# Kernel tuning notes

Hardware: AMD Instinct MI355X
Metric: run time of the kernel (lower is better)

Reference implementation:

```python
import jax, jax.numpy as jnp
import numpy as np

ALPHA = 300.0   # attractor_alpha
N_ATT = 16      # n_attractors
MIN_D = 0.001
MAX_D = 10.0


def _resize_bilinear_ac(x, out_h, out_w):
    """Bilinear resize with align_corners=True on trailing (H, W) dims of [B,C,h,w]."""
    h, w = x.shape[-2], x.shape[-1]
    ys = jnp.arange(out_h, dtype=jnp.float32) * ((h - 1) / max(out_h - 1, 1))
    xs = jnp.arange(out_w, dtype=jnp.float32) * ((w - 1) / max(out_w - 1, 1))
    y0 = jnp.floor(ys).astype(jnp.int32); y1 = jnp.minimum(y0 + 1, h - 1)
    x0 = jnp.floor(xs).astype(jnp.int32); x1 = jnp.minimum(x0 + 1, w - 1)
    wy = (ys - y0.astype(jnp.float32))[:, None]   # [out_h, 1]
    wx = (xs - x0.astype(jnp.float32))[None, :]   # [1, out_w]
    v00 = x[..., y0[:, None], x0[None, :]]
    v01 = x[..., y0[:, None], x1[None, :]]
    v10 = x[..., y1[:, None], x0[None, :]]
    v11 = x[..., y1[:, None], x1[None, :]]
    top = v00 * (1 - wx) + v01 * wx
    bot = v10 * (1 - wx) + v11 * wx
    return top * (1 - wy) + bot * wy


def setup_inputs() -> dict:
    key = jax.random.key(0)
    k = jax.random.split(key, 7)
    B, C, H, W = 4, 128, 192, 192
    n_bins = 64
    x = jax.random.normal(k[0], (B, C, H, W), dtype=jnp.float32)
    prev_bin = jax.random.uniform(k[1], (B, n_bins, H // 2, W // 2), dtype=jnp.float32)
    prev_bin_embedding = jax.random.normal(k[2], (B, C, H // 2, W // 2), dtype=jnp.float32)
    w1 = jax.random.normal(k[3], (128, 128), dtype=jnp.float32) * 0.05
    b1 = jnp.zeros((128,), dtype=jnp.float32)
    w2 = jax.random.normal(k[4], (2 * N_ATT, 128), dtype=jnp.float32) * 0.05
    b2 = jnp.zeros((2 * N_ATT,), dtype=jnp.float32)
    return {"x": x, "prev_bin": prev_bin, "prev_bin_embedding": prev_bin_embedding,
            "w1": w1, "b1": b1, "w2": w2, "b2": b2}


def reference(x, prev_bin, prev_bin_embedding, w1, b1, w2, b2):
    B, C, H, W = x.shape
    # add (interpolated) previous bin embedding
    pe = _resize_bilinear_ac(prev_bin_embedding, H, W)
    h = x + pe
    # per-pixel MLP (two 1x1 convs)
    h = jax.nn.relu(jnp.einsum('bchw,oc->bohw', h, w1) + b1[:, None, None])
    att = jax.nn.relu(jnp.einsum('bchw,oc->bohw', h, w2) + b2[:, None, None]) + 0.001
    # [B, n_attractors, 2, H, W] -> take normed attractor points
    att = att.reshape(B, N_ATT, 2, H, W)[:, :, 0]          # [B, nA, H, W]
    # upsample previous bin centers to feature resolution
    bc = _resize_bilinear_ac(prev_bin, H, W)               # [B, nB, H, W]
    # broadcast-subtract + inverse attractor + mean over attractors
    dx = att[:, :, None, :, :] - bc[:, None, :, :, :]      # [B, nA, nB, H, W]
    delta_c = jnp.mean(dx / (1.0 + ALPHA * dx * dx), axis=1)  # gamma = 2
    bin_new_centers = bc + delta_c
    bin_centers = (MAX_D - MIN_D) * bin_new_centers + MIN_D
    bin_centers = jnp.clip(jnp.sort(bin_centers, axis=1), MIN_D, MAX_D)
    return bin_new_centers, bin_centers
```

## Files before the change

### kernel.cpp

```cpp
#include <hip/hip_runtime.h>

constexpr int Bc = 4, Cc = 128, Hc = 192, Wc = 192;
constexpr int HI = 96, WI = 96;
constexpr int NB = 64;
constexpr int NA = 16;
constexpr float SCL = 95.0f / 191.0f;

typedef __attribute__((ext_vector_type(8))) short bf16x8;
typedef __attribute__((ext_vector_type(4))) float f32x4;

__device__ __forceinline__ unsigned short f2bf(float f) {
  unsigned u = __builtin_bit_cast(unsigned, f);
  unsigned r = (u + 0x7FFFu + ((u >> 16) & 1u)) >> 16;
  return (unsigned short)r;
}
__device__ __forceinline__ float rcp_fast(float r) {
#if defined(__has_builtin)
#if __has_builtin(__builtin_amdgcn_rcpf)
  return __builtin_amdgcn_rcpf(r);
#else
  return 1.0f / r;
#endif
#else
  return 1.0f / r;
#endif
}

__global__ __launch_bounds__(256) void k_prep(
    const float* __restrict__ w1, const float* __restrict__ w2,
    unsigned short* __restrict__ w1bf, unsigned short* __restrict__ w2bf)
{
  const int t = blockIdx.x * 256 + threadIdx.x;
  if (t < 16384) {
    w1bf[t] = f2bf(w1[t]);
  } else {
    const int u = t - 16384;
    const int j = u >> 7, c = u & 127;
    w2bf[u] = f2bf(w2[(2 * j) * 128 + c]);
  }
}

__global__ __launch_bounds__(256, 8) void k_att(
    const float* __restrict__ x, const float* __restrict__ pbe,
    const unsigned short* __restrict__ w1bf, const float* __restrict__ b1,
    const unsigned short* __restrict__ w2bf, const float* __restrict__ b2,
    float* __restrict__ att)
{
  constexpr int PH = 136;
  constexpr int RP = 37;
  __shared__ __align__(16) unsigned char smem[128 * RP * 4];
  float*          row_s = (float*)smem;
  unsigned short* a1_s  = (unsigned short*)smem;

  const int tid = threadIdx.x;
  const int xg0 = blockIdx.x * 64;
  const int y = blockIdx.y;
  const int b = blockIdx.z;

  const float ysf = y * SCL;
  const int y0 = (int)ysf;
  const int y1 = min(y0 + 1, HI - 1);
  const float wy = ysf - (float)y0;
  const int xi0 = (int)(xg0 * SCL);

  const int lane = tid & 63;
  const int wv = tid >> 6;
  const int ln = lane & 15;
  const int qd = lane >> 4;
  const int m0 = wv * 16;

  const int px = m0 + ln;
  const int xg = xg0 + px;
  const float xsf = (float)xg * SCL;
  const int x0i = (int)xsf;
  const float wx = xsf - (float)x0i;
  const int xl = x0i - xi0;

  float xr[32];
  #pragma unroll
  for (int kt = 0; kt < 4; ++kt) {
    #pragma unroll
    for (int j = 0; j < 8; ++j) {
      const int c = kt * 32 + qd * 8 + j;
      xr[kt * 8 + j] = x[((size_t)(b * Cc + c) * Hc + y) * Wc + xg];
    }
  }

  #pragma unroll
  for (int i = 0; i < 18; ++i) {
    const int f = tid + 256 * i;
    const int c = f / 36;
    const int xi = f - c * 36;
    const int xgl = min(xi0 + xi, WI - 1);
    const float* p = pbe + (size_t)(b * Cc + c) * (HI * WI);
    const float top = p[y0 * WI + xgl];
    const float bot = p[y1 * WI + xgl];
    row_s[c * RP + xi] = top + wy * (bot - top);
  }
  __syncthreads();

  bf16x8 af[4];
  #pragma unroll
  for (int kt = 0; kt < 4; ++kt) {
    #pragma unroll
    for (int j = 0; j < 8; ++j) {
      const int c = kt * 32 + qd * 8 + j;
      const float v0 = row_s[c * RP + xl];
      const float v1 = row_s[c * RP + xl + 1];
      af[kt][j] = (short)f2bf(xr[kt * 8 + j] + v0 + wx * (v1 - v0));
    }
  }
  __syncthreads();

  f32x4 acc[8];
  #pragma unroll
  for (int nt = 0; nt < 8; ++nt) acc[nt] = f32x4{0.f, 0.f, 0.f, 0.f};
  #pragma unroll
  for (int nt = 0; nt < 8; ++nt) {
    #pragma unroll
    for (int kt = 0; kt < 4; ++kt) {
      const bf16x8 bf = *(const bf16x8*)&w1bf[(nt * 16 + ln) * 128 + kt * 32 + qd * 8];
      acc[nt] = __builtin_amdgcn_mfma_f32_16x16x32_bf16(af[kt], bf, acc[nt], 0, 0, 0);
    }
  }

  #pragma unroll
  for (int nt = 0; nt < 8; ++nt) {
    const int n = nt * 16 + ln;
    const float bias = b1[n];
    #pragma unroll
    for (int r = 0; r < 4; ++r) {
      const int m = m0 + qd * 4 + r;
      a1_s[m * PH + n] = f2bf(fmaxf(acc[nt][r] + bias, 0.f));
    }
  }

  f32x4 acc2 = f32x4{0.f, 0.f, 0.f, 0.f};
  #pragma unroll
  for (int kt = 0; kt < 4; ++kt) {
    const bf16x8 a2 = *(const bf16x8*)&a1_s[(m0 + ln) * PH + kt * 32 + qd * 8];
    const bf16x8 b2f = *(const bf16x8*)&w2bf[ln * 128 + kt * 32 + qd * 8];
    acc2 = __builtin_amdgcn_mfma_f32_16x16x32_bf16(a2, b2f, acc2, 0, 0, 0);
  }
  const float bias2 = b2[2 * ln];
  #pragma unroll
  for (int r = 0; r < 4; ++r) {
    const int opx = m0 + qd * 4 + r;
    const float v = fmaxf(acc2[r] + bias2, 0.f) + 0.001f;
    att[((size_t)((b * Hc + y) * Wc) + xg0 + opx) * NA + ln] = v;
  }
}

__global__ __launch_bounds__(192, 2) void k_bins(
    const float* __restrict__ pb, const float* __restrict__ att,
    float* __restrict__ out0, float* __restrict__ out1)
{
  __shared__ __align__(16) float row_s[NB][WI];

  const int tid = threadIdx.x;
  const int y = blockIdx.x;
  const int b = blockIdx.y;

  const float ysf = y * SCL;
  const int y0 = (int)ysf;
  const int y1 = min(y0 + 1, HI - 1);
  const float wy = ysf - (float)y0;

  float am[16];
  {
    const float4* ap = (const float4*)(att + ((size_t)((b * Hc + y) * Wc) + tid) * NA);
    const float4 a0 = ap[0], a1 = ap[1], a2 = ap[2], a3 = ap[3];
    am[0] = a0.x;  am[1] = a0.y;  am[2] = a0.z;  am[3] = a0.w;
    am[4] = a1.x;  am[5] = a1.y;  am[6] = a1.z;  am[7] = a1.w;
    am[8] = a2.x;  am[9] = a2.y;  am[10] = a2.z; am[11] = a2.w;
    am[12] = a3.x; am[13] = a3.y; am[14] = a3.z; am[15] = a3.w;
  }

  #pragma unroll
  for (int i = 0; i < 8; ++i) {
    const int u = tid + 192 * i;
    const int k = u / 24;
    const int g = u - k * 24;
    const float* base = pb + (size_t)(b * NB + k) * (HI * WI);
    const float4 t4 = *(const float4*)&base[y0 * WI + g * 4];
    const float4 b4 = *(const float4*)&base[y1 * WI + g * 4];
    float4 r;
    r.x = t4.x + wy * (b4.x - t4.x);
    r.y = t4.y + wy * (b4.y - t4.y);
    r.z = t4.z + wy * (b4.z - t4.z);
    r.w = t4.w + wy * (b4.w - t4.w);
    *(float4*)&row_s[k][g * 4] = r;
  }
  __syncthreads();

  const float xsf = tid * SCL;
  const int x0 = (int)xsf;
  const float wx = xsf - (float)x0;

  const size_t obase = (size_t)(b * NB) * (Hc * Wc) + (size_t)y * Wc + tid;
  float v[NB];

  #pragma unroll
  for (int kb = 0; kb < NB; kb += 4) {
    float bc[4], dl[4];
    #pragma unroll
    for (int q = 0; q < 4; ++q) {
      const int k = kb + q;
      const float v0 = row_s[k][x0], v1 = row_s[k][x0 + 1];
      bc[q] = v0 + wx * (v1 - v0);
      dl[q] = 0.f;
    }
    #pragma unroll
    for (int j = 0; j < NA; ++j) {
      const float a = am[j];
      #pragma unroll
      for (int q = 0; q < 4; ++q) {
        const float d = a - bc[q];
        const float rq = fmaf(300.f * d, d, 1.f);
        dl[q] = fmaf(d, rcp_fast(rq), dl[q]);
      }
    }
    #pragma unroll
    for (int q = 0; q < 4; ++q) {
      const float bnc = fmaf(dl[q], 1.f / 16.f, bc[q]);
      out0[obase + (size_t)(kb + q) * (Hc * Wc)] = bnc;
      v[kb + q] = fmaf(9.999f, bnc, 0.001f);
    }
  }

  #pragma unroll
  for (int size = 2; size <= NB; size <<= 1) {
    #pragma unroll
    for (int stride = size >> 1; stride >= 1; stride >>= 1) {
      #pragma unroll
      for (int i = 0; i < NB; ++i) {
        if ((i & stride) == 0) {
          const int j = i | stride;
          const bool asc = ((i & size) == 0);
          const float a = v[i], c = v[j];
          const float lo = fminf(a, c), hi = fmaxf(a, c);
          v[i] = asc ? lo : hi;
          v[j] = asc ? hi : lo;
        }
      }
    }
  }

  #pragma unroll
  for (int k = 0; k < NB; ++k) {
    out1[obase + (size_t)k * (Hc * Wc)] = fminf(fmaxf(v[k], 0.001f), 10.0f);
  }
}

extern "C" void kernel_launch(void* const* d_in, const int* in_sizes, int n_in,
                              void* d_out, int out_size, void* d_ws, size_t ws_size,
                              hipStream_t stream) {
  const float* x   = (const float*)d_in[0];
  const float* pb  = (const float*)d_in[1];
  const float* pbe = (const float*)d_in[2];
  const float* w1  = (const float*)d_in[3];
  const float* b1  = (const float*)d_in[4];
  const float* w2  = (const float*)d_in[5];
  const float* b2  = (const float*)d_in[6];

  float* out0 = (float*)d_out;
  float* out1 = out0 + (size_t)Bc * NB * Hc * Wc;

  unsigned short* w1bf = (unsigned short*)d_ws;
  unsigned short* w2bf = w1bf + 16384;
  float* att = (float*)((char*)d_ws + 65536);

  k_prep<<<72, 256, 0, stream>>>(w1, w2, w1bf, w2bf);

  dim3 g1(Wc / 64, Hc, Bc);
  k_att<<<g1, 256, 0, stream>>>(x, pbe, w1bf, b1, w2bf, b2, att);

  dim3 g2(Hc, Bc);
  k_bins<<<g2, 192, 0, stream>>>(pb, att, out0, out1);
}
```

Before: 256.0 us.

## Pre-swizzle bf16 weights into MFMA fragment order and stage W1 in LDS

The prep kernel now writes W1 and the selected W2 rows in per-lane MFMA fragment order, so each lane reads one contiguous 16-byte chunk. k_att copies all of W1 into 32 KB of shared memory once per block and reads its B fragments from there instead of making scattered global loads. W2 fragments and the biases are hoisted into registers. This adds LDS per block and more live registers, and lowers the occupancy hint from 8 to 3, which may reduce latency hiding for the x and pbe loads.

```diff
diff --git a/kernel.cpp b/kernel.cpp
--- a/kernel.cpp
+++ b/kernel.cpp
@@ -28,29 +28,40 @@
 
 __global__ __launch_bounds__(256) void k_prep(
     const float* __restrict__ w1, const float* __restrict__ w2,
-    unsigned short* __restrict__ w1bf, unsigned short* __restrict__ w2bf)
+    unsigned short* __restrict__ w1p, unsigned short* __restrict__ w2p)
 {
   const int t = blockIdx.x * 256 + threadIdx.x;
   if (t < 16384) {
-    w1bf[t] = f2bf(w1[t]);
+    const int e  = t & 7;
+    const int l  = (t >> 3) & 63;
+    const int kt = (t >> 9) & 3;
+    const int nt = t >> 11;
+    const int n  = nt * 16 + (l & 15);
+    const int k  = kt * 32 + (l >> 4) * 8 + e;
+    w1p[t] = f2bf(w1[n * 128 + k]);
   } else {
-    const int u = t - 16384;
-    const int j = u >> 7, c = u & 127;
-    w2bf[u] = f2bf(w2[(2 * j) * 128 + c]);
-  }
-}
-
-__global__ __launch_bounds__(256, 8) void k_att(
+    const int u  = t - 16384;
+    const int e  = u & 7;
+    const int l  = (u >> 3) & 63;
+    const int kt = u >> 9;
+    const int n  = 2 * (l & 15);
+    const int k  = kt * 32 + (l >> 4) * 8 + e;
+    w2p[u] = f2bf(w2[n * 128 + k]);
+  }
+}
+
+__global__ __launch_bounds__(256, 3) void k_att(
     const float* __restrict__ x, const float* __restrict__ pbe,
-    const unsigned short* __restrict__ w1bf, const float* __restrict__ b1,
-    const unsigned short* __restrict__ w2bf, const float* __restrict__ b2,
+    const unsigned short* __restrict__ w1p, const float* __restrict__ b1,
+    const unsigned short* __restrict__ w2p, const float* __restrict__ b2,
     float* __restrict__ att)
 {
   constexpr int PH = 136;
   constexpr int RP = 37;
-  __shared__ __align__(16) unsigned char smem[128 * RP * 4];
-  float*          row_s = (float*)smem;
-  unsigned short* a1_s  = (unsigned short*)smem;
+  __shared__ __align__(16) unsigned char smem[32768 + 128 * RP * 4];
+  unsigned short* w1_s  = (unsigned short*)smem;
+  float*          row_s = (float*)(smem + 32768);
+  unsigned short* a1_s  = (unsigned short*)(smem + 32768);
 
   const int tid = threadIdx.x;
   const int xg0 = blockIdx.x * 64;
@@ -75,6 +86,22 @@
   const int x0i = (int)xsf;
   const float wx = xsf - (float)x0i;
   const int xl = x0i - xi0;
+
+  float4 wstage[8];
+  {
+    const float4* wp4 = (const float4*)w1p;
+    #pragma unroll
+    for (int i = 0; i < 8; ++i) wstage[i] = wp4[tid + 256 * i];
+  }
+
+  bf16x8 b2f[4];
+  #pragma unroll
+  for (int kt = 0; kt < 4; ++kt)
+    b2f[kt] = *(const bf16x8*)&w2p[kt * 512 + lane * 8];
+  float bias1[8];
+  #pragma unroll
+  for (int nt = 0; nt < 8; ++nt) bias1[nt] = b1[nt * 16 + ln];
+  const float bias2 = b2[2 * ln];
 
   float xr[32];
   #pragma unroll
@@ -97,6 +124,12 @@
     const float bot = p[y1 * WI + xgl];
     row_s[c * RP + xi] = top + wy * (bot - top);
   }
+
+  {
+    float4* ws4 = (float4*)w1_s;
+    #pragma unroll
+    for (int i = 0; i < 8; ++i) ws4[tid + 256 * i] = wstage[i];
+  }
   __syncthreads();
 
   bf16x8 af[4];
@@ -119,7 +152,7 @@
   for (int nt = 0; nt < 8; ++nt) {
     #pragma unroll
     for (int kt = 0; kt < 4; ++kt) {
-      const bf16x8 bf = *(const bf16x8*)&w1bf[(nt * 16 + ln) * 128 + kt * 32 + qd * 8];
+      const bf16x8 bf = *(const bf16x8*)&w1_s[(nt * 4 + kt) * 512 + lane * 8];
       acc[nt] = __builtin_amdgcn_mfma_f32_16x16x32_bf16(af[kt], bf, acc[nt], 0, 0, 0);
     }
   }
@@ -127,7 +160,7 @@
   #pragma unroll
   for (int nt = 0; nt < 8; ++nt) {
     const int n = nt * 16 + ln;
-    const float bias = b1[n];
+    const float bias = bias1[nt];
     #pragma unroll
     for (int r = 0; r < 4; ++r) {
       const int m = m0 + qd * 4 + r;
@@ -139,10 +172,8 @@
   #pragma unroll
   for (int kt = 0; kt < 4; ++kt) {
     const bf16x8 a2 = *(const bf16x8*)&a1_s[(m0 + ln) * PH + kt * 32 + qd * 8];
-    const bf16x8 b2f = *(const bf16x8*)&w2bf[ln * 128 + kt * 32 + qd * 8];
-    acc2 = __builtin_amdgcn_mfma_f32_16x16x32_bf16(a2, b2f, acc2, 0, 0, 0);
-  }
-  const float bias2 = b2[2 * ln];
+    acc2 = __builtin_amdgcn_mfma_f32_16x16x32_bf16(a2, b2f[kt], acc2, 0, 0, 0);
+  }
   #pragma unroll
   for (int r = 0; r < 4; ++r) {
     const int opx = m0 + qd * 4 + r;
@@ -266,14 +297,14 @@
   float* out0 = (float*)d_out;
   float* out1 = out0 + (size_t)Bc * NB * Hc * Wc;
 
-  unsigned short* w1bf = (unsigned short*)d_ws;
-  unsigned short* w2bf = w1bf + 16384;
+  unsigned short* w1p = (unsigned short*)d_ws;
+  unsigned short* w2p = w1p + 16384;
   float* att = (float*)((char*)d_ws + 65536);
 
-  k_prep<<<72, 256, 0, stream>>>(w1, w2, w1bf, w2bf);
+  k_prep<<<72, 256, 0, stream>>>(w1, w2, w1p, w2p);
 
   dim3 g1(Wc / 64, Hc, Bc);
-  k_att<<<g1, 256, 0, stream>>>(x, pbe, w1bf, b1, w2bf, b2, att);
+  k_att<<<g1, 256, 0, stream>>>(x, pbe, w1p, b1, w2p, b2, att);
 
   dim3 g2(Hc, Bc);
   k_bins<<<g2, 192, 0, stream>>>(pb, att, out0, out1);
```

After: 217.3 us. 1.18x faster.
